# Optimization experiments

Measured on AMD Instinct MI355X. Metric: run time of the kernel, lower is better.

Reference implementation:

```python
import jax, jax.numpy as jnp
import numpy as np

EPS_MAG = 1e-6    # magnitude threshold for valid trajectory
EPS_WSUM = 1e-8   # clamp on combined weight sum


def setup_inputs() -> dict:
    key = jax.random.key(0)
    embeddings = jax.random.normal(key, (4, 4096, 1024), dtype=jnp.float32)
    return {"embeddings": embeddings, "max_trajectory_distance": 8}


def reference(embeddings, max_trajectory_distance):
    # Vectorized form of compute_sparse_trajectories:
    # for each pos p >= 1, window of diffs d[start..p-1], start = max(0, p - max_dist),
    # normalized diffs weighted by linspace(0.1, 1.0, window) * tanh(2*|d|),
    # output[p] = weighted sum / clamp(weight sum, 1e-8); output[0] = 0.
    B, S, D = embeddings.shape
    maxd = min(int(max_trajectory_distance), S - 1)

    d = embeddings[:, 1:, :] - embeddings[:, :-1, :]            # [B, S-1, D]
    mag = jnp.linalg.norm(d, axis=-1)                           # [B, S-1]
    normed = jnp.where((mag > EPS_MAG)[..., None],
                       d / jnp.maximum(mag, EPS_MAG)[..., None],
                       0.0)                                     # [B, S-1, D]
    magw = jnp.tanh(mag * 2.0)                                  # [B, S-1]

    p = jnp.arange(S)                                           # positions
    wsize = jnp.minimum(maxd, p)                                # window size per pos
    j = jnp.arange(maxd)
    idx = p[:, None] - maxd + j[None, :]                        # [S, maxd] diff indices (end-aligned)
    valid = idx >= 0                                            # [S, maxd]
    # k = rank within window (0..wsize-1): weights linspace(0.1, 1.0, wsize)
    k = (j[None, :] - (maxd - wsize)[:, None]).astype(jnp.float32)
    denom = jnp.maximum(wsize - 1, 1).astype(jnp.float32)[:, None]
    lin = jnp.where(wsize[:, None] > 1, 0.1 + 0.9 * k / denom, 0.1)
    lin = jnp.where(valid, lin, 0.0)                            # [S, maxd]

    ci = jnp.clip(idx, 0, S - 2)                                # safe gather indices
    n_g = normed[:, ci, :]                                      # [B, S, maxd, D]
    m_g = magw[:, ci]                                           # [B, S, maxd]
    comb = lin[None, :, :] * m_g * valid[None, :, :]            # combined weights

    wsum = jnp.maximum(comb.sum(axis=-1), EPS_WSUM)             # [B, S]
    traj = jnp.einsum('bsjd,bsj->bsd', n_g, comb) / wsum[..., None]
    return traj
```

## Files before the change

kernel.cpp:

```cpp
#include <hip/hip_runtime.h>
#include <hip/hip_bf16.h>


constexpr int B_ = 4;
constexpr int S_ = 4096;
constexpr int D_ = 1024;
constexpr int MAXD  = 8;
constexpr int CHUNK = 16;
constexpr int ROWS  = CHUNK + MAXD;
constexpr int NDIFF = ROWS - 1;

__global__ __launch_bounds__(256)
void traj_splat_kernel(const float* __restrict__ emb, float* __restrict__ out) {
    const int s0   = blockIdx.x * CHUNK;
    const int b    = blockIdx.y;
    const int lane = threadIdx.x & 63;
    const int wave = threadIdx.x >> 6;
    const int d0   = threadIdx.x * 4;

    const float* __restrict__ embB = emb + (size_t)b * S_ * D_;

    __shared__ float part[NDIFF][4];
    __shared__ float smagw[NDIFF];
    __shared__ float sq[NDIFF];
    __shared__ float gco[CHUNK][MAXD + 1];

    float4 win[ROWS];
    #pragma unroll
    for (int r = 0; r < ROWS; ++r) {
        const int row = s0 - MAXD + r;
        if (row >= 0)
            win[r] = *(const float4*)(embB + (size_t)row * D_ + d0);
        else
            win[r] = make_float4(0.f, 0.f, 0.f, 0.f);
    }

    #pragma unroll
    for (int li = 0; li < NDIFF; ++li) {
        const float4 a = win[li], c = win[li + 1];
        const float dx = c.x - a.x, dy = c.y - a.y;
        const float dz = c.z - a.z, dw = c.w - a.w;
        float sum = dx * dx + dy * dy + dz * dz + dw * dw;
        #pragma unroll
        for (int off = 32; off >= 1; off >>= 1)
            sum += __shfl_xor(sum, off, 64);
        if (lane == 0) part[li][wave] = sum;
    }
    __syncthreads();

    if (threadIdx.x < NDIFF) {
        const int li = threadIdx.x;
        const float s2  = part[li][0] + part[li][1] + part[li][2] + part[li][3];
        const float mag = sqrtf(s2);
        const float mw  = tanhf(2.f * mag);
        smagw[li] = mw;
        sq[li]    = (mag > 1e-6f) ? (mw / mag) : 0.f;
    }
    __syncthreads();

    if (threadIdx.x < CHUNK) {
        const int sl = threadIdx.x;
        const int s  = s0 + sl;
        const int ws = min(MAXD, s);
        const int lo = MAXD - ws;
        const float rden = 0.9f / (float)max(ws - 1, 1);

        float cpad[MAXD + 2];
        #pragma unroll
        for (int t = 0; t < MAXD + 2; ++t) cpad[t] = 0.f;

        float wsum = 0.f;
        #pragma unroll
        for (int j = 0; j < MAXD; ++j) {
            if (j >= lo) {
                const int li = sl + j;
                const float lin = (ws > 1) ? (0.1f + rden * (float)(j - lo)) : 0.1f;
                wsum += lin * smagw[li];
                cpad[j + 1] = lin * sq[li];
            }
        }
        const float inv = 1.f / fmaxf(wsum, 1e-8f);
        #pragma unroll
        for (int jr = 0; jr <= MAXD; ++jr)
            gco[sl][jr] = (cpad[jr] - cpad[jr + 1]) * inv;
    }
    __syncthreads();

    #pragma unroll
    for (int sl = 0; sl < CHUNK; ++sl) {
        float4 acc = make_float4(0.f, 0.f, 0.f, 0.f);
        #pragma unroll
        for (int jr = 0; jr <= MAXD; ++jr) {
            const float g = gco[sl][jr];
            acc.x += g * win[sl + jr].x;
            acc.y += g * win[sl + jr].y;
            acc.z += g * win[sl + jr].z;
            acc.w += g * win[sl + jr].w;
        }
        *(float4*)(out + ((size_t)b * S_ + s0 + sl) * D_ + d0) = acc;
    }
}

extern "C" void kernel_launch(void* const* d_in, const int* in_sizes, int n_in,
                              void* d_out, int out_size, void* d_ws, size_t ws_size,
                              hipStream_t stream) {
    const float* emb = (const float*)d_in[0];
    float* out = (float*)d_out;

    dim3 grid(S_ / CHUNK, B_);
    dim3 block(256);
    traj_splat_kernel<<<grid, block, 0, stream>>>(emb, out);
}
```

Before: 31.42 us.

## Double chunk size, remap blocks across XCDs, vectorize coefficient loads

Raises the rows per block from 16 to 32, which cuts the halo re-read overhead from 8/16 to 8/32 of each chunk. A 1D grid with an XCD-aware block remap keeps neighbouring chunks on the same XCD to share L2. The warp reduction is shortened to four shuffles with partial sums written to LDS, and coefficients are read as padded float4. The larger register window (40 float4) risks register pressure and lower occupancy, even with launch bounds set to 2 blocks.

```diff
diff --git a/kernel.cpp b/kernel.cpp
--- a/kernel.cpp
+++ b/kernel.cpp
@@ -6,24 +6,31 @@
 constexpr int S_ = 4096;
 constexpr int D_ = 1024;
 constexpr int MAXD  = 8;
-constexpr int CHUNK = 16;
+constexpr int CHUNK = 32;
 constexpr int ROWS  = CHUNK + MAXD;
 constexpr int NDIFF = ROWS - 1;
+constexpr int NCHUNK = S_ / CHUNK;
+constexpr int NWG    = NCHUNK * B_;
+constexpr int NXCD   = 8;
 
-__global__ __launch_bounds__(256)
+__global__ __launch_bounds__(256, 2)
 void traj_splat_kernel(const float* __restrict__ emb, float* __restrict__ out) {
-    const int s0   = blockIdx.x * CHUNK;
-    const int b    = blockIdx.y;
+    const int bid = blockIdx.x;
+    const int lin = (bid % NXCD) * (NWG / NXCD) + bid / NXCD;
+    const int schunk = lin & (NCHUNK - 1);
+    const int b      = lin >> 7;
+
+    const int s0   = schunk * CHUNK;
     const int lane = threadIdx.x & 63;
     const int wave = threadIdx.x >> 6;
     const int d0   = threadIdx.x * 4;
 
     const float* __restrict__ embB = emb + (size_t)b * S_ * D_;
 
-    __shared__ float part[NDIFF][4];
+    __shared__ float part[NDIFF][4][4];
     __shared__ float smagw[NDIFF];
     __shared__ float sq[NDIFF];
-    __shared__ float gco[CHUNK][MAXD + 1];
+    __shared__ float gco[CHUNK][12];
 
     float4 win[ROWS];
     #pragma unroll
@@ -41,16 +48,22 @@
         const float dx = c.x - a.x, dy = c.y - a.y;
         const float dz = c.z - a.z, dw = c.w - a.w;
         float sum = dx * dx + dy * dy + dz * dz + dw * dw;
-        #pragma unroll
-        for (int off = 32; off >= 1; off >>= 1)
-            sum += __shfl_xor(sum, off, 64);
-        if (lane == 0) part[li][wave] = sum;
+        sum += __shfl_xor(sum, 32, 64);
+        sum += __shfl_xor(sum, 16, 64);
+        sum += __shfl_xor(sum,  8, 64);
+        sum += __shfl_xor(sum,  4, 64);
+        if (lane < 4) part[li][wave][lane] = sum;
     }
     __syncthreads();
 
     if (threadIdx.x < NDIFF) {
         const int li = threadIdx.x;
-        const float s2  = part[li][0] + part[li][1] + part[li][2] + part[li][3];
+        float s2 = 0.f;
+        #pragma unroll
+        for (int w = 0; w < 4; ++w)
+            #pragma unroll
+            for (int k = 0; k < 4; ++k)
+                s2 += part[li][w][k];
         const float mag = sqrtf(s2);
         const float mw  = tanhf(2.f * mag);
         smagw[li] = mw;
@@ -74,9 +87,9 @@
         for (int j = 0; j < MAXD; ++j) {
             if (j >= lo) {
                 const int li = sl + j;
-                const float lin = (ws > 1) ? (0.1f + rden * (float)(j - lo)) : 0.1f;
-                wsum += lin * smagw[li];
-                cpad[j + 1] = lin * sq[li];
+                const float lin2 = (ws > 1) ? (0.1f + rden * (float)(j - lo)) : 0.1f;
+                wsum += lin2 * smagw[li];
+                cpad[j + 1] = lin2 * sq[li];
             }
         }
         const float inv = 1.f / fmaxf(wsum, 1e-8f);
@@ -86,18 +99,26 @@
     }
     __syncthreads();
 
+    float* outB = out + ((size_t)b * S_ + s0) * D_ + d0;
     #pragma unroll
     for (int sl = 0; sl < CHUNK; ++sl) {
-        float4 acc = make_float4(0.f, 0.f, 0.f, 0.f);
+        const float4 g0 = *(const float4*)&gco[sl][0];
+        const float4 g1 = *(const float4*)&gco[sl][4];
+        const float  g8 = gco[sl][8];
+
+        float4 acc;
+        acc.x = g0.x * win[sl].x; acc.y = g0.x * win[sl].y;
+        acc.z = g0.x * win[sl].z; acc.w = g0.x * win[sl].w;
+        const float gs[8] = {g0.y, g0.z, g0.w, g1.x, g1.y, g1.z, g1.w, g8};
         #pragma unroll
-        for (int jr = 0; jr <= MAXD; ++jr) {
-            const float g = gco[sl][jr];
+        for (int jr = 1; jr <= MAXD; ++jr) {
+            const float g = gs[jr - 1];
             acc.x += g * win[sl + jr].x;
             acc.y += g * win[sl + jr].y;
             acc.z += g * win[sl + jr].z;
             acc.w += g * win[sl + jr].w;
         }
-        *(float4*)(out + ((size_t)b * S_ + s0 + sl) * D_ + d0) = acc;
+        *(float4*)(outB + (size_t)sl * D_) = acc;
     }
 }
 
@@ -107,7 +128,7 @@
     const float* emb = (const float*)d_in[0];
     float* out = (float*)d_out;
 
-    dim3 grid(S_ / CHUNK, B_);
+    dim3 grid(NWG);
     dim3 block(256);
     traj_splat_kernel<<<grid, block, 0, stream>>>(emb, out);
 }
```

Result: faster. 29.71 us (-5.4%).
